# Optimization experiments

Hardware: AMD Instinct MI355X
Metric: run time of the kernel (lower is better)

## Reference

```python
import jax, jax.numpy as jnp
import numpy as np
import math

L = 8           # n_layers
DIM = 1024
H = 16          # num_heads
HD = DIM // H   # head_dim
HID = 4096      # mlp hidden
V = 32000       # vocab
B, T = 2, 1024


def setup_inputs() -> dict:
    key = jax.random.key(0)
    ks = jax.random.split(key, 10)
    s = 0.02
    inp = {
        "input_ids": jax.random.randint(ks[0], (B, T), 0, V, dtype=jnp.int32),
        "labels": jax.random.randint(ks[1], (B, T), 0, V, dtype=jnp.int32),
        "Wemb": jax.random.normal(ks[2], (V, DIM), jnp.float32) * s,   # tied embed / lm_head
        "Wq": jax.random.normal(ks[3], (L, DIM, DIM), jnp.float32) * s,
        "Wk": jax.random.normal(ks[4], (L, DIM, DIM), jnp.float32) * s,
        "Wv": jax.random.normal(ks[5], (L, DIM, DIM), jnp.float32) * s,
        "Wo": jax.random.normal(ks[6], (L, DIM, DIM), jnp.float32) * s,
        "Wfc": jax.random.normal(ks[7], (L, DIM, HID), jnp.float32) * s,
        "Wgate": jax.random.normal(ks[8], (L, DIM, HID), jnp.float32) * s,
        "Wproj": jax.random.normal(ks[9], (L, HID, DIM), jnp.float32) * s,
    }
    return inp


def _forward(input_ids, labels, Wemb, Wq, Wk, Wv, Wo, Wfc, Wgate, Wproj):
    b, t = input_ids.shape
    h = Wemb[input_ids]                                   # [B,T,C] embedding lookup
    # causal additive mask: -inf strictly above diagonal
    mask = jnp.triu(jnp.full((t, t), -jnp.inf, dtype=h.dtype), k=1)
    inv_sqrt_L = 1.0 / math.sqrt(L)
    inv_sqrt_hd = 1.0 / math.sqrt(HD)
    inv_sqrt_hid = 1.0 / math.sqrt(HID)

    def block(h, params):
        wq, wk, wv, wo, wfc, wgate, wproj = params
        # attention (explicit QK^T softmax V, as in source)
        q = (h @ wq).reshape(b, t, H, HD)
        k = (h @ wk).reshape(b, t, H, HD)
        v = (h @ wv).reshape(b, t, H, HD)
        scores = jnp.einsum("bqhd,bkhd->bhqk", q, k) * inv_sqrt_hd + mask
        probs = jax.nn.softmax(scores, axis=-1)
        attn = jnp.einsum("bhqk,bkhd->bqhd", probs, v).reshape(b, t, DIM)
        h = h + (attn @ wo) * inv_sqrt_L
        # SwiGLU MLP with 1/sqrt(hidden) scaling
        mlp = (((h @ wfc) * jax.nn.silu(h @ wgate)) * inv_sqrt_hid) @ wproj
        h = h + mlp * inv_sqrt_L
        return h, None

    h, _ = jax.lax.scan(block, h, (Wq, Wk, Wv, Wo, Wfc, Wgate, Wproj))

    logits = h @ Wemb.T                                   # tied lm_head [B,T,V]
    # cross entropy with ignore_index=-1
    lab = labels.reshape(-1)
    valid = lab != -1
    safe = jnp.where(valid, lab, 0)
    logp = jax.nn.log_softmax(logits.reshape(-1, V), axis=-1)
    nll = -jnp.take_along_axis(logp, safe[:, None], axis=-1)[:, 0]
    loss = jnp.sum(jnp.where(valid, nll, 0.0)) / jnp.maximum(jnp.sum(valid), 1)
    return logits, loss


def reference(input_ids, labels, Wemb, Wq, Wk, Wv, Wo, Wfc, Wgate, Wproj):
    return _forward(input_ids, labels, Wemb, Wq, Wk, Wv, Wo, Wfc, Wgate, Wproj)
```

## Files before the change

kernel.cpp:

```cpp
#include <hip/hip_runtime.h>
#include <hip/hip_bf16.h>
#include <math.h>

#define L_LAYERS 8
#define DIM 1024
#define NH 16
#define HD 64
#define HID 4096
#define VOCAB 32000
#define BB 2
#define TT 1024
#define MROWS (BB*TT)

typedef unsigned short u16;
typedef short short8 __attribute__((ext_vector_type(8)));
typedef float f32x4 __attribute__((ext_vector_type(4)));
typedef unsigned short us4 __attribute__((ext_vector_type(4)));
typedef unsigned short us8 __attribute__((ext_vector_type(8)));

__device__ __forceinline__ float bf2f(u16 x){
  union { unsigned int u; float f; } v; v.u = ((unsigned int)x) << 16; return v.f;
}
__device__ __forceinline__ u16 f2bf(float f){
  union { float f; unsigned int u; } v; v.f = f;
  unsigned int r = (v.u + 0x7fffu + ((v.u >> 16) & 1u)) >> 16; return (u16)r;
}

#define AS1 __attribute__((address_space(1)))
#define AS3 __attribute__((address_space(3)))
__device__ __forceinline__ void gld_lds16(const void* g, void* l){
  __builtin_amdgcn_global_load_lds((const AS1 void*)g, (AS3 void*)l, 16, 0, 0);
}

__global__ void k_embed(const int* __restrict__ ids, const float* __restrict__ Wemb,
                        float* __restrict__ h, u16* __restrict__ hb){
  int bt = blockIdx.x; long id = ids[bt];
  const float4* src = (const float4*)(Wemb + id*(long)DIM);
  float4 v = src[threadIdx.x];
  ((float4*)(h + (long)bt*DIM))[threadIdx.x] = v;
  us4 o = { f2bf(v.x), f2bf(v.y), f2bf(v.z), f2bf(v.w) };
  ((us4*)(hb + (long)bt*DIM))[threadIdx.x] = o;
}

__global__ void k_cvt(const float* __restrict__ src, u16* __restrict__ dst, long n){
  long i = ((long)blockIdx.x*256 + threadIdx.x)*8;
  if (i >= n) return;
  float4 a = ((const float4*)(src+i))[0];
  float4 b = ((const float4*)(src+i))[1];
  us4 o0 = { f2bf(a.x), f2bf(a.y), f2bf(a.z), f2bf(a.w) };
  us4 o1 = { f2bf(b.x), f2bf(b.y), f2bf(b.z), f2bf(b.w) };
  ((us4*)(dst+i))[0] = o0; ((us4*)(dst+i))[1] = o1;
}

__global__ void k_cvt_layer(const float* __restrict__ Wq, const float* __restrict__ Wk,
    const float* __restrict__ Wv, const float* __restrict__ Wo,
    const float* __restrict__ Wfc, const float* __restrict__ Wg, const float* __restrict__ Wp,
    u16* __restrict__ qkvT, u16* __restrict__ woT, u16* __restrict__ fgT, u16* __restrict__ projT)
{
  int tile = blockIdx.x;
  const float* src; u16* dst; int R, C, tr, tc;
  long rowmul = 1, rowoff = 0;
  if (tile < 1024){
    int m = tile >> 8, t2 = tile & 255;
    tr = t2 >> 4; tc = t2 & 15; R = 1024; C = 1024;
    src = (m==0)?Wq:(m==1)?Wk:(m==2)?Wv:Wo;
    dst = (m<3)? qkvT + (long)m*1024*1024 : woT;
  } else if (tile < 3072){
    int m = (tile - 1024) >> 10, t2 = (tile - 1024) & 1023;
    tr = t2 >> 6; tc = t2 & 63; R = 1024; C = 4096;
    src = m ? Wg : Wfc; dst = fgT; rowmul = 2; rowoff = m;
  } else {
    int t2 = tile - 3072;
    tr = t2 >> 4; tc = t2 & 15; R = 4096; C = 1024;
    src = Wp; dst = projT;
  }
  __shared__ float ls[64][65];
  int u = threadIdx.x;
  int rr16 = u >> 4;
  int cu   = u & 15;
  #pragma unroll
  for (int p = 0; p < 4; ++p){
    int r = p*16 + rr16;
    float4 v = *(const float4*)(src + (long)(tr*64 + r)*C + tc*64 + cu*4);
    ls[r][cu*4+0]=v.x; ls[r][cu*4+1]=v.y; ls[r][cu*4+2]=v.z; ls[r][cu*4+3]=v.w;
  }
  __syncthreads();
  int d  = u >> 2;
  int c4 = u & 3;
  long drow = (long)tc*64 + d;
  u16* dp = dst + (drow*rowmul + rowoff)*R + tr*64;
  #pragma unroll
  for (int g2 = 0; g2 < 2; ++g2){
    int e0 = (c4 + g2*4) * 8;
    us8 o;
    #pragma unroll
    for (int j=0;j<8;j++) o[j] = f2bf(ls[e0+j][d]);
    *((us8*)(dp + e0)) = o;
  }
}

template<int EPI>
__global__ __launch_bounds__(256, 2) void k_gemm(
    const u16* __restrict__ A, long lda,
    const u16* __restrict__ Bt, long ldb,
    void* __restrict__ Cp, long ldc,
    int K, int nMt, float alpha, int ksplit,
    u16* __restrict__ hbout)
{
  __shared__ u16 lsA[128*32];
  __shared__ u16 lsB[128*32];
  int nflat = gridDim.x; int w = blockIdx.x;
  if ((nflat & 7) == 0){ int q = nflat >> 3; w = (w & 7)*q + (w >> 3); }
  int perk = nflat / ksplit;
  int kc = w / perk; int w2 = w - kc*perk;
  int mtile = w2 % nMt, ntile = w2 / nMt;
  const u16* Ab = A + (long)mtile*128*lda + (long)kc*K;
  const u16* Bb = Bt + (long)ntile*128*ldb + (long)kc*K;
  int t = threadIdx.x;
  int wv = t >> 6, ln = t & 63;
  int srow = t >> 2;
  int scol = (t & 3) * 8;
  int fr = ln & 15, kg = ln >> 4;
  int wr = wv >> 1, wc = wv & 1;
  const f32x4 zero = {0.f,0.f,0.f,0.f};
  f32x4 acc[4][4];
  #pragma unroll
  for (int m=0;m<4;m++)
    #pragma unroll
    for (int n=0;n<4;n++) acc[m][n] = zero;
  const u16* ga0 = Ab + (long)srow*lda + scol;
  const u16* ga1 = Ab + (long)(srow+64)*lda + scol;
  const u16* gb0 = Bb + (long)srow*ldb + scol;
  const u16* gb1 = Bb + (long)(srow+64)*ldb + scol;
  u16* la0 = lsA + wv*512;
  u16* la1 = lsA + 2048 + wv*512;
  u16* lb0 = lsB + wv*512;
  u16* lb1 = lsB + 2048 + wv*512;
  for (int k0 = 0; k0 < K; k0 += 32){
    gld_lds16(ga0 + k0, la0);
    gld_lds16(ga1 + k0, la1);
    gld_lds16(gb0 + k0, lb0);
    gld_lds16(gb1 + k0, lb1);
    __syncthreads();
    short8 af[4], bfr[4];
    #pragma unroll
    for (int m=0;m<4;m++) af[m]  = *(const short8*)(lsA + (wr*64 + m*16 + fr)*32 + kg*8);
    #pragma unroll
    for (int n=0;n<4;n++) bfr[n] = *(const short8*)(lsB + (wc*64 + n*16 + fr)*32 + kg*8);
    #pragma unroll
    for (int m=0;m<4;m++)
      #pragma unroll
      for (int n=0;n<4;n++)
        acc[m][n] = __builtin_amdgcn_mfma_f32_16x16x32_bf16(af[m], bfr[n], acc[m][n], 0, 0, 0);
    __syncthreads();
  }
  long row0 = (long)mtile*128 + wr*64 + kg*4;
  int col0 = ntile*128 + wc*64 + fr;
  if constexpr (EPI == 0){
    u16* C = (u16*)Cp;
    #pragma unroll
    for (int m=0;m<4;m++)
      #pragma unroll
      for (int r=0;r<4;r++){
        long row = row0 + m*16 + r;
        #pragma unroll
        for (int n=0;n<4;n++) C[row*ldc + col0 + n*16] = f2bf(acc[m][n][r]);
      }
  } else if constexpr (EPI == 2){
    float* C = (float*)Cp;
    #pragma unroll
    for (int m=0;m<4;m++)
      #pragma unroll
      for (int r=0;r<4;r++){
        long row = row0 + m*16 + r;
        #pragma unroll
        for (int n=0;n<4;n++){
          long idx = row*ldc + col0 + n*16;
          float v = C[idx] + acc[m][n][r]*alpha;
          C[idx] = v;
          hbout[idx] = f2bf(v);
        }
      }
  } else {
    float* C = (float*)Cp + (long)kc*MROWS*ldc;
    #pragma unroll
    for (int m=0;m<4;m++)
      #pragma unroll
      for (int r=0;r<4;r++){
        long row = row0 + m*16 + r;
        #pragma unroll
        for (int n=0;n<4;n++) C[row*ldc + col0 + n*16] = acc[m][n][r];
      }
  }
}

template<int NS>
__global__ void k_redKn(const float* __restrict__ pK, float* __restrict__ h, u16* __restrict__ hb){
  long idx = ((long)blockIdx.x*256 + threadIdx.x)*4;
  const float aL = 0.35355339059327373f;
  float4 s = *(const float4*)(pK + idx);
  #pragma unroll
  for (int j=1;j<NS;j++){
    float4 sj = *(const float4*)(pK + idx + (long)j*MROWS*1024);
    s.x += sj.x; s.y += sj.y; s.z += sj.z; s.w += sj.w;
  }
  float4 hv = *(const float4*)(h + idx);
  float4 v;
  v.x = hv.x + s.x*aL;
  v.y = hv.y + s.y*aL;
  v.z = hv.z + s.z*aL;
  v.w = hv.w + s.w*aL;
  *(float4*)(h + idx) = v;
  us4 o = { f2bf(v.x), f2bf(v.y), f2bf(v.z), f2bf(v.w) };
  *(us4*)(hb + idx) = o;
}

#define MFMA_(va,vb,vc) __builtin_amdgcn_mfma_f32_16x16x32_bf16(va,vb,vc,0,0,0)
#define RD2(base, row, ku) (*(const short8*)((base) + (row)*64 + ((((ku) ^ ((row)&7)))<<3)))

template<int EPI>
__global__ __launch_bounds__(512, 1) void k_gemm256(
    const u16* __restrict__ A, long lda,
    const u16* __restrict__ Bt, long ldb,
    void* __restrict__ Cp, long ldc,
    int K, int nMt,
    float2* __restrict__ partials)
{
  __shared__ u16 lds[65536];
  int nwg = gridDim.x; int w = blockIdx.x;
  { int q = nwg >> 3, r8 = nwg & 7; int xcd = w & 7, lw = w >> 3;
    w = (xcd < r8 ? xcd*(q+1) : r8*(q+1) + (xcd-r8)*q) + lw; }
  int mtile = w % nMt, ntile = w / nMt;
  const u16* Abase = A + (long)mtile*256*lda;
  const u16* Bbase = Bt + (long)ntile*256*ldb;
  int tid = threadIdx.x;
  int wid = tid >> 6, ln = tid & 63;
  int wm = wid >> 2, wn = wid & 3;
  int fr = ln & 15, kg = ln >> 4;

  f32x4 acc[8][4];
  #pragma unroll
  for (int a=0;a<8;a++)
    #pragma unroll
    for (int b=0;b<4;b++) acc[a][b] = (f32x4){0.f,0.f,0.f,0.f};

#define STAGE_A(i, kofs, dstbase) do{ \
    int u_ = (i)*512 + tid; int r_ = u_>>3; int cu_ = u_&7; \
    gld_lds16(Abase + (long)r_*lda + (kofs) + ((cu_^(r_&7))<<3), \
              (dstbase) + (((i)*512 + wid*64)<<3)); }while(0)
#define STAGE_B(i, kofs, dstbase) do{ \
    int u_ = (i)*512 + tid; int r_ = u_>>3; int cu_ = u_&7; \
    gld_lds16(Bbase + (long)r_*ldb + (kofs) + ((cu_^(r_&7))<<3), \
              (dstbase) + (((i)*512 + wid*64)<<3)); }while(0)

#define KHALF(ks) do{ \
    short8 a0 = RD2(ldsA, wm*128 +   0 + fr, (ks)*4+kg); \
    short8 a1 = RD2(ldsA, wm*128 +  16 + fr, (ks)*4+kg); \
    short8 a2 = RD2(ldsA, wm*128 +  32 + fr, (ks)*4+kg); \
    short8 a3 = RD2(ldsA, wm*128 +  48 + fr, (ks)*4+kg); \
    short8 a4 = RD2(ldsA, wm*128 +  64 + fr, (ks)*4+kg); \
    short8 a5 = RD2(ldsA, wm*128 +  80 + fr, (ks)*4+kg); \
    short8 a6 = RD2(ldsA, wm*128 +  96 + fr, (ks)*4+kg); \
    short8 a7 = RD2(ldsA, wm*128 + 112 + fr, (ks)*4+kg); \
    short8 b0 = RD2(ldsB, wn*64 +  0 + fr, (ks)*4+kg); \
    short8 b1 = RD2(ldsB, wn*64 + 16 + fr, (ks)*4+kg); \
    short8 b2 = RD2(ldsB, wn*64 + 32 + fr, (ks)*4+kg); \
    short8 b3 = RD2(ldsB, wn*64 + 48 + fr, (ks)*4+kg); \
    acc[0][0]=MFMA_(a0,b0,acc[0][0]); acc[1][0]=MFMA_(a1,b0,acc[1][0]); \
    acc[0][1]=MFMA_(a0,b1,acc[0][1]); acc[1][1]=MFMA_(a1,b1,acc[1][1]); \
    acc[2][0]=MFMA_(a2,b0,acc[2][0]); acc[3][0]=MFMA_(a3,b0,acc[3][0]); \
    acc[2][1]=MFMA_(a2,b1,acc[2][1]); acc[3][1]=MFMA_(a3,b1,acc[3][1]); \
    acc[0][2]=MFMA_(a0,b2,acc[0][2]); acc[1][2]=MFMA_(a1,b2,acc[1][2]); \
    acc[0][3]=MFMA_(a0,b3,acc[0][3]); acc[1][3]=MFMA_(a1,b3,acc[1][3]); \
    acc[2][2]=MFMA_(a2,b2,acc[2][2]); acc[3][2]=MFMA_(a3,b2,acc[3][2]); \
    acc[2][3]=MFMA_(a2,b3,acc[2][3]); acc[3][3]=MFMA_(a3,b3,acc[3][3]); \
    acc[4][0]=MFMA_(a4,b0,acc[4][0]); acc[5][0]=MFMA_(a5,b0,acc[5][0]); \
    acc[4][1]=MFMA_(a4,b1,acc[4][1]); acc[5][1]=MFMA_(a5,b1,acc[5][1]); \
    acc[6][0]=MFMA_(a6,b0,acc[6][0]); acc[7][0]=MFMA_(a7,b0,acc[7][0]); \
    acc[6][1]=MFMA_(a6,b1,acc[6][1]); acc[7][1]=MFMA_(a7,b1,acc[7][1]); \
    acc[4][2]=MFMA_(a4,b2,acc[4][2]); acc[5][2]=MFMA_(a5,b2,acc[5][2]); \
    acc[4][3]=MFMA_(a4,b3,acc[4][3]); acc[5][3]=MFMA_(a5,b3,acc[5][3]); \
    acc[6][2]=MFMA_(a6,b2,acc[6][2]); acc[7][2]=MFMA_(a7,b2,acc[7][2]); \
    acc[6][3]=MFMA_(a6,b3,acc[6][3]); acc[7][3]=MFMA_(a7,b3,acc[7][3]); \
  }while(0)

  {
    u16* dA = lds; u16* dB = lds + 16384;
    STAGE_A(0, 0, dA); STAGE_A(1, 0, dA); STAGE_A(2, 0, dA); STAGE_A(3, 0, dA);
    STAGE_B(0, 0, dB); STAGE_B(1, 0, dB); STAGE_B(2, 0, dB); STAGE_B(3, 0, dB);
  }
  const int NT = K >> 6;
  #pragma unroll 2
  for (int jt = 0; jt < NT; ++jt){
    int bsel = jt & 1;
    u16* ldsA = lds + bsel*32768;
    u16* ldsB = ldsA + 16384;
    u16* nA = lds + (bsel^1)*32768;
    u16* nB = nA + 16384;
    long k1 = (long)(jt+1) << 6;
    bool pref = (jt+1 < NT);
    if (pref){
      STAGE_A(0, k1, nA); STAGE_A(1, k1, nA);
      STAGE_B(0, k1, nB); STAGE_B(1, k1, nB);
      asm volatile("s_waitcnt vmcnt(4)" ::: "memory");
    } else {
      asm volatile("s_waitcnt vmcnt(0)" ::: "memory");
    }
    __builtin_amdgcn_s_barrier();
    __builtin_amdgcn_s_setprio(1);
    KHALF(0);
    __builtin_amdgcn_s_setprio(0);
    __builtin_amdgcn_sched_barrier(0);
    if (pref){
      STAGE_A(2, k1, nA); STAGE_A(3, k1, nA);
      STAGE_B(2, k1, nB); STAGE_B(3, k1, nB);
    }
    __builtin_amdgcn_sched_barrier(0);
    __builtin_amdgcn_s_setprio(1);
    KHALF(1);
    __builtin_amdgcn_s_setprio(0);
    __builtin_amdgcn_sched_barrier(0);
    __builtin_amdgcn_s_barrier();
  }

  if constexpr (EPI == 3){
    u16* act = (u16*)Cp;
    const float sc = 0.015625f;
    #pragma unroll
    for (int a=0;a<8;a++){
      long rowb = (long)mtile*256 + wm*128 + a*16 + kg*4;
      #pragma unroll
      for (int r=0;r<4;r++){
        #pragma unroll
        for (int b=0;b<4;b++){
          float v = acc[a][b][r];
          float pv = __shfl_xor(v, 1);
          if (!(fr & 1)){
            int colg = ntile*256 + wn*64 + b*16 + fr;
            float g = pv;
            float sl = g / (1.0f + __expf(-g));
            act[(rowb+r)*ldc + (colg>>1)] = f2bf(v * sl * sc);
          }
        }
      }
    }
  } else {
    float* C = (float*)Cp;
    #pragma unroll
    for (int a=0;a<8;a++){
      long rowb = (long)mtile*256 + wm*128 + a*16 + kg*4;
      #pragma unroll
      for (int r=0;r<4;r++){
        #pragma unroll
        for (int b=0;b<4;b++){
          int colg = ntile*256 + wn*64 + b*16 + fr;
          C[(rowb+r)*ldc + colg] = acc[a][b][r];
        }
      }
    }
    float* pm = (float*)lds;
    float* ps = pm + 1024;
    #pragma unroll
    for (int a=0;a<8;a++)
      #pragma unroll
      for (int r=0;r<4;r++){
        float M = fmaxf(fmaxf(acc[a][0][r],acc[a][1][r]), fmaxf(acc[a][2][r],acc[a][3][r]));
        #pragma unroll
        for (int o=1;o<16;o<<=1) M = fmaxf(M, __shfl_xor(M, o));
        float S = __expf(acc[a][0][r]-M) + __expf(acc[a][1][r]-M)
                + __expf(acc[a][2][r]-M) + __expf(acc[a][3][r]-M);
        #pragma unroll
        for (int o=1;o<16;o<<=1) S += __shfl_xor(S, o);
        if (fr == 0){
          int rl = wm*128 + a*16 + kg*4 + r;
          pm[wn*256 + rl] = M; ps[wn*256 + rl] = S;
        }
      }
    __syncthreads();
    if (tid < 256){
      float m0 = pm[tid], m1 = pm[256+tid], m2 = pm[512+tid], m3 = pm[768+tid];
      float M = fmaxf(fmaxf(m0,m1), fmaxf(m2,m3));
      float S = ps[tid]*__expf(m0-M) + ps[256+tid]*__expf(m1-M)
              + ps[512+tid]*__expf(m2-M) + ps[768+tid]*__expf(m3-M);
      partials[((long)mtile*256 + tid)*128 + ntile] = make_float2(M, S);
    }
  }
#undef STAGE_A
#undef STAGE_B
#undef KHALF
}

__global__ void k_transpose_v(const u16* __restrict__ qkv, u16* __restrict__ vT){
  int ttile = blockIdx.x; int z = blockIdx.y;
  long b = z >> 4; int hh = z & 15;
  const u16* v = qkv + b*TT*3072 + 2048 + hh*64;
  u16* outp = vT + (long)z*64*TT;
  __shared__ u16 ls[64][65];
  int u = threadIdx.x, rr = u & 63, cc = u >> 6;
  const u16* sp = v + (long)(ttile*64 + rr)*3072 + cc*16;
  us4 a0 = ((const us4*)sp)[0];
  us4 a1 = ((const us4*)sp)[1];
  us4 a2 = ((const us4*)sp)[2];
  us4 a3 = ((const us4*)sp)[3];
  #pragma unroll
  for (int j=0;j<4;j++){ ls[rr][cc*16+j] = a0[j]; ls[rr][cc*16+4+j] = a1[j];
                         ls[rr][cc*16+8+j] = a2[j]; ls[rr][cc*16+12+j] = a3[j]; }
  __syncthreads();
  int d = u & 63;
  #pragma unroll
  for (int g=0; g<4; ++g){
    int tl = cc*16 + g*4;
    int t  = ttile*64 + tl;
    int ut = (t >> 3) & 15;
    int tp = (t & ~127) + (((ut ^ (d & 15)) << 3) | (t & 7));
    us4 o = { ls[tl+0][d], ls[tl+1][d], ls[tl+2][d], ls[tl+3][d] };
    *((us4*)(outp + (long)d*TT + tp)) = o;
  }
}

__global__ __launch_bounds__(128) void k_flash(
    const u16* __restrict__ qkv, const u16* __restrict__ vT, u16* __restrict__ attnb)
{
  __shared__ u16 lsQ[64*64];
  __shared__ u16 lsK[128*64];
  __shared__ u16 lsV[64*128];
  __shared__ u16 lsP[64*128];
  int id = blockIdx.x;
  int wq = id >> 5, z = id & 31;
  int qt = (wq < 8) ? wq : 23 - wq;
  long bT = (long)(z >> 4) * TT;
  int h64 = (z & 15) * 64;
  int t = threadIdx.x, wv = t >> 6, ln = t & 63;
  int fr = ln & 15, kg = ln >> 4;
  const u16* vbase = vT + (long)z*64*TT;

  #pragma unroll
  for (int p=0; p<4; ++p){
    int r = p*16 + wv*8 + (ln>>3);
    const u16* g = qkv + (bT + qt*64 + r)*3072 + h64 + (((ln&7) ^ (ln>>3))*8);
    gld_lds16(g, lsQ + (p*16 + wv*8)*64);
  }

  f32x4 S[2][8], O[2][4];
  float Mst[2][4], Lst[2][4];
  #pragma unroll
  for (int m=0;m<2;m++){
    #pragma unroll
    for (int n=0;n<4;n++) O[m][n] = (f32x4){0.f,0.f,0.f,0.f};
    #pragma unroll
    for (int r=0;r<4;r++){ Mst[m][r] = -3.0e38f; Lst[m][r] = 0.f; }
  }

  int nk = (qt >> 1) + 1;
  for (int kt = 0; kt < nk; ++kt){
    #pragma unroll
    for (int p=0; p<8; ++p){
      int r = p*16 + wv*8 + (ln>>3);
      const u16* g = qkv + (bT + kt*128 + r)*3072 + 1024 + h64 + (((ln&7) ^ (ln>>3))*8);
      gld_lds16(g, lsK + (p*16 + wv*8)*64);
    }
    #pragma unroll
    for (int p=0; p<8; ++p){
      int d = p*8 + wv*4 + (ln>>4);
      const u16* g = vbase + (long)d*TT + kt*128 + (ln&15)*8;
      gld_lds16(g, lsV + (p*8 + wv*4)*128);
    }
    __syncthreads();

    #pragma unroll
    for (int m=0;m<2;m++)
      #pragma unroll
      for (int n=0;n<8;n++) S[m][n] = (f32x4){0.f,0.f,0.f,0.f};
    #pragma unroll
    for (int ks=0; ks<2; ++ks){
      int un = ((ks*4 + kg) ^ (fr & 7)) * 8;
      short8 a0 = *(const short8*)(lsQ + (wv*32 +      fr)*64 + un);
      short8 a1 = *(const short8*)(lsQ + (wv*32 + 16 + fr)*64 + un);
      #pragma unroll
      for (int n=0;n<8;n++){
        short8 bb = *(const short8*)(lsK + (n*16 + fr)*64 + un);
        S[0][n] = __builtin_amdgcn_mfma_f32_16x16x32_bf16(a0, bb, S[0][n], 0,0,0);
        S[1][n] = __builtin_amdgcn_mfma_f32_16x16x32_bf16(a1, bb, S[1][n], 0,0,0);
      }
    }

    #pragma unroll
    for (int m=0;m<2;m++){
      #pragma unroll
      for (int r=0;r<4;r++){
        int rloc = wv*32 + m*16 + kg*4 + r;
        int row_g = qt*64 + rloc;
        float x[8]; float mx = -3.0e38f;
        #pragma unroll
        for (int n=0;n<8;n++){
          int col_g = kt*128 + n*16 + fr;
          x[n] = (col_g <= row_g) ? S[m][n][r]*0.125f : -3.0e38f;
          mx = fmaxf(mx, x[n]);
        }
        #pragma unroll
        for (int o=1;o<16;o<<=1) mx = fmaxf(mx, __shfl_xor(mx, o));
        float Mnew = fmaxf(Mst[m][r], mx);
        float corr = __expf(Mst[m][r] - Mnew);
        Mst[m][r] = Mnew;
        float s = 0.f;
        #pragma unroll
        for (int n=0;n<8;n++){
          float p = __expf(x[n] - Mnew);
          s += p;
          int col = n*16 + fr;
          int col2 = ((((col>>3) ^ (rloc & 15)) << 3) | (col & 7));
          lsP[rloc*128 + col2] = f2bf(p);
        }
        #pragma unroll
        for (int o=1;o<16;o<<=1) s += __shfl_xor(s, o);
        Lst[m][r] = Lst[m][r]*corr + s;
        #pragma unroll
        for (int n=0;n<4;n++) O[m][n][r] *= corr;
      }
    }

    #pragma unroll
    for (int ks=0; ks<4; ++ks){
      int up = ((ks*4 + kg) ^ fr) * 8;
      short8 p0 = *(const short8*)(lsP + (wv*32 +      fr)*128 + up);
      short8 p1 = *(const short8*)(lsP + (wv*32 + 16 + fr)*128 + up);
      #pragma unroll
      for (int n=0;n<4;n++){
        short8 vb = *(const short8*)(lsV + (n*16 + fr)*128 + up);
        O[0][n] = __builtin_amdgcn_mfma_f32_16x16x32_bf16(p0, vb, O[0][n], 0,0,0);
        O[1][n] = __builtin_amdgcn_mfma_f32_16x16x32_bf16(p1, vb, O[1][n], 0,0,0);
      }
    }
    __syncthreads();
  }

  #pragma unroll
  for (int m=0;m<2;m++)
    #pragma unroll
    for (int r=0;r<4;r++){
      float inv = 1.0f / Lst[m][r];
      long row = bT + qt*64 + wv*32 + m*16 + kg*4 + r;
      #pragma unroll
      for (int n=0;n<4;n++)
        attnb[row*1024 + h64 + n*16 + fr] = f2bf(O[m][n][r]*inv);
    }
}

__global__ void k_nll2(const float2* __restrict__ part, const float* __restrict__ logits,
                       const int* __restrict__ labels, float* __restrict__ nll){
  int row = blockIdx.x; int ln = threadIdx.x;
  const float2* pr = part + (long)row*128;
  float m = -3.0e38f, s = 0.f;
  for (int j = ln; j < 125; j += 64){
    float2 p = pr[j];
    float M = fmaxf(m, p.x);
    s = s*__expf(m - M) + p.y*__expf(p.x - M);
    m = M;
  }
  #pragma unroll
  for (int o=32;o;o>>=1){
    float om = __shfl_xor(m, o), os = __shfl_xor(s, o);
    float M = fmaxf(m, om);
    s = s*__expf(m - M) + os*__expf(om - M);
    m = M;
  }
  if (ln == 0){
    int lab = labels[row];
    float lse = m + __logf(s);
    nll[row] = (lab != -1) ? (lse - logits[(long)row*VOCAB + lab]) : 0.f;
  }
}

__global__ void k_loss(const float* __restrict__ nll, const int* __restrict__ labels,
                       float* __restrict__ out){
  int tid = threadIdx.x;
  int wv = tid >> 6;
  float s = 0.f; float c = 0.f;
  for (int i = tid; i < MROWS; i += 256){
    s += nll[i];
    c += (labels[i] != -1) ? 1.f : 0.f;
  }
  #pragma unroll
  for (int o=32;o;o>>=1){ s += __shfl_xor(s, o); c += __shfl_xor(c, o); }
  __shared__ float rsm[4], rc[4];
  if ((tid & 63) == 0){ rsm[wv] = s; rc[wv] = c; }
  __syncthreads();
  if (tid == 0){
    s = rsm[0]+rsm[1]+rsm[2]+rsm[3];
    c = rc[0]+rc[1]+rc[2]+rc[3];
    out[(long)MROWS*VOCAB] = s / fmaxf(c, 1.f);
  }
}

extern "C" void kernel_launch(void* const* d_in, const int* in_sizes, int n_in,
                              void* d_out, int out_size, void* d_ws, size_t ws_size,
                              hipStream_t stream)
{
  (void)in_sizes; (void)n_in; (void)out_size; (void)ws_size;
  const int*   ids    = (const int*)d_in[0];
  const int*   labels = (const int*)d_in[1];
  const float* Wemb   = (const float*)d_in[2];
  const float* Wq     = (const float*)d_in[3];
  const float* Wk     = (const float*)d_in[4];
  const float* Wv     = (const float*)d_in[5];
  const float* Wo     = (const float*)d_in[6];
  const float* Wfc    = (const float*)d_in[7];
  const float* Wg     = (const float*)d_in[8];
  const float* Wp     = (const float*)d_in[9];
  float* logits = (float*)d_out;

  char* ws = (char*)d_ws;
  size_t off = 0;
  auto alloc = [&](size_t bytes){ void* p = ws + off; off += (bytes + 255) & ~(size_t)255; return p; };
  u16*    wembBf = (u16*)alloc((size_t)VOCAB*DIM*2);
  float*  h      = (float*)alloc((size_t)MROWS*DIM*4);
  u16*    hb     = (u16*)alloc((size_t)MROWS*DIM*2);
  u16*    qkvT   = (u16*)alloc((size_t)3*DIM*DIM*2);
  u16*    woT    = (u16*)alloc((size_t)DIM*DIM*2);
  u16*    fgT    = (u16*)alloc((size_t)2*HID*DIM*2);
  u16*    projT  = (u16*)alloc((size_t)DIM*HID*2);
  u16*    qkv    = (u16*)alloc((size_t)MROWS*3*DIM*2);
  u16*    vT     = (u16*)alloc((size_t)BB*NH*64*TT*2);
  u16*    attnb  = (u16*)alloc((size_t)MROWS*DIM*2);
  u16*    act    = (u16*)alloc((size_t)MROWS*HID*2);
  float*  pK     = (float*)alloc((size_t)4*MROWS*DIM*4);
  float2* parts  = (float2*)alloc((size_t)MROWS*128*8);
  float*  nllb   = (float*)alloc((size_t)MROWS*4);

  dim3 blk(256,1,1);
  dim3 blk512(512,1,1);
  const float aL = 0.35355339059327373f;

  k_cvt<<<dim3(16000,1,1),blk,0,stream>>>(Wemb, wembBf, (long)VOCAB*DIM);
  k_embed<<<dim3(MROWS,1,1),blk,0,stream>>>(ids, Wemb, h, hb);

  for (int l = 0; l < L_LAYERS; ++l){
    k_cvt_layer<<<dim3(4096,1,1),blk,0,stream>>>(
        Wq + (size_t)l*DIM*DIM, Wk + (size_t)l*DIM*DIM, Wv + (size_t)l*DIM*DIM, Wo + (size_t)l*DIM*DIM,
        Wfc + (size_t)l*DIM*HID, Wg + (size_t)l*DIM*HID, Wp + (size_t)l*HID*DIM,
        qkvT, woT, fgT, projT);
    k_gemm<0><<<dim3(384,1,1),blk,0,stream>>>(hb,1024, qkvT,1024, qkv,3072,
        1024,16,1.f,1, nullptr);
    k_transpose_v<<<dim3(16,32,1),blk,0,stream>>>(qkv, vT);
    k_flash<<<dim3(512,1,1),dim3(128,1,1),0,stream>>>(qkv, vT, attnb);
    k_gemm<5><<<dim3(256,1,1),blk,0,stream>>>(attnb,1024, woT,1024, pK,1024,
        512,16,1.f,2, nullptr);
    k_redKn<2><<<dim3(2048,1,1),blk,0,stream>>>(pK, h, hb);
    k_gemm256<3><<<dim3(256,1,1),blk512,0,stream>>>(hb,1024, fgT,1024, act,4096,
        1024,8, nullptr);
    k_gemm<5><<<dim3(512,1,1),blk,0,stream>>>(act,4096, projT,4096, pK,1024,
        1024,16,1.f,4, nullptr);
    k_redKn<4><<<dim3(2048,1,1),blk,0,stream>>>(pK, h, hb);
  }
  k_gemm256<4><<<dim3(1000,1,1),blk512,0,stream>>>(hb,1024, wembBf,1024, logits,32000,
      1024,8, parts);
  k_nll2<<<dim3(MROWS,1,1),dim3(64,1,1),0,stream>>>(parts, logits, labels, nllb);
  k_loss<<<dim3(1,1,1),blk,0,stream>>>(nllb, labels, logits);
}
```

Baseline: 1.808 ms.

## Shrink flash-attention query tile to 32 rows and alias P buffer onto K

The flash attention kernel now handles 32 query rows per block instead of 64, so the grid doubles to 1024 blocks with one 16-row MFMA strip per wave. The P buffer reuses the K shared-memory region, with an extra barrier after QK^T. The goal is higher occupancy, less LDS and fewer registers per block, plus better balance of causal work across blocks. The cost is that every K/V tile is loaded twice as often, since fewer query rows share each load, and each iteration gains a synchronisation.

```diff
diff --git a/kernel.cpp b/kernel.cpp
--- a/kernel.cpp
+++ b/kernel.cpp
@@ -421,13 +421,13 @@
 __global__ __launch_bounds__(128) void k_flash(
     const u16* __restrict__ qkv, const u16* __restrict__ vT, u16* __restrict__ attnb)
 {
-  __shared__ u16 lsQ[64*64];
+  __shared__ u16 lsQ[32*64];
   __shared__ u16 lsK[128*64];
   __shared__ u16 lsV[64*128];
-  __shared__ u16 lsP[64*128];
+  u16* lsP = lsK;
   int id = blockIdx.x;
   int wq = id >> 5, z = id & 31;
-  int qt = (wq < 8) ? wq : 23 - wq;
+  int qt = (wq < 16) ? wq : 47 - wq;
   long bT = (long)(z >> 4) * TT;
   int h64 = (z & 15) * 64;
   int t = threadIdx.x, wv = t >> 6, ln = t & 63;
@@ -435,23 +435,20 @@
   const u16* vbase = vT + (long)z*64*TT;
 
   #pragma unroll
-  for (int p=0; p<4; ++p){
+  for (int p=0; p<2; ++p){
     int r = p*16 + wv*8 + (ln>>3);
-    const u16* g = qkv + (bT + qt*64 + r)*3072 + h64 + (((ln&7) ^ (ln>>3))*8);
+    const u16* g = qkv + (bT + qt*32 + r)*3072 + h64 + (((ln&7) ^ (ln>>3))*8);
     gld_lds16(g, lsQ + (p*16 + wv*8)*64);
   }
 
-  f32x4 S[2][8], O[2][4];
-  float Mst[2][4], Lst[2][4];
-  #pragma unroll
-  for (int m=0;m<2;m++){
-    #pragma unroll
-    for (int n=0;n<4;n++) O[m][n] = (f32x4){0.f,0.f,0.f,0.f};
-    #pragma unroll
-    for (int r=0;r<4;r++){ Mst[m][r] = -3.0e38f; Lst[m][r] = 0.f; }
-  }
-
-  int nk = (qt >> 1) + 1;
+  f32x4 S[8], O[4];
+  float Mst[4], Lst[4];
+  #pragma unroll
+  for (int n=0;n<4;n++) O[n] = (f32x4){0.f,0.f,0.f,0.f};
+  #pragma unroll
+  for (int r=0;r<4;r++){ Mst[r] = -3.0e38f; Lst[r] = 0.f; }
+
+  int nk = (qt >> 2) + 1;
   for (int kt = 0; kt < nk; ++kt){
     #pragma unroll
     for (int p=0; p<8; ++p){
@@ -468,82 +465,72 @@
     __syncthreads();
 
     #pragma unroll
-    for (int m=0;m<2;m++)
-      #pragma unroll
-      for (int n=0;n<8;n++) S[m][n] = (f32x4){0.f,0.f,0.f,0.f};
+    for (int n=0;n<8;n++) S[n] = (f32x4){0.f,0.f,0.f,0.f};
     #pragma unroll
     for (int ks=0; ks<2; ++ks){
       int un = ((ks*4 + kg) ^ (fr & 7)) * 8;
-      short8 a0 = *(const short8*)(lsQ + (wv*32 +      fr)*64 + un);
-      short8 a1 = *(const short8*)(lsQ + (wv*32 + 16 + fr)*64 + un);
+      short8 a0 = *(const short8*)(lsQ + (wv*16 + fr)*64 + un);
       #pragma unroll
       for (int n=0;n<8;n++){
         short8 bb = *(const short8*)(lsK + (n*16 + fr)*64 + un);
-        S[0][n] = __builtin_amdgcn_mfma_f32_16x16x32_bf16(a0, bb, S[0][n], 0,0,0);
-        S[1][n] = __builtin_amdgcn_mfma_f32_16x16x32_bf16(a1, bb, S[1][n], 0,0,0);
-      }
-    }
-
-    #pragma unroll
-    for (int m=0;m<2;m++){
-      #pragma unroll
-      for (int r=0;r<4;r++){
-        int rloc = wv*32 + m*16 + kg*4 + r;
-        int row_g = qt*64 + rloc;
-        float x[8]; float mx = -3.0e38f;
-        #pragma unroll
-        for (int n=0;n<8;n++){
-          int col_g = kt*128 + n*16 + fr;
-          x[n] = (col_g <= row_g) ? S[m][n][r]*0.125f : -3.0e38f;
-          mx = fmaxf(mx, x[n]);
-        }
-        #pragma unroll
-        for (int o=1;o<16;o<<=1) mx = fmaxf(mx, __shfl_xor(mx, o));
-        float Mnew = fmaxf(Mst[m][r], mx);
-        float corr = __expf(Mst[m][r] - Mnew);
-        Mst[m][r] = Mnew;
-        float s = 0.f;
-        #pragma unroll
-        for (int n=0;n<8;n++){
-          float p = __expf(x[n] - Mnew);
-          s += p;
-          int col = n*16 + fr;
-          int col2 = ((((col>>3) ^ (rloc & 15)) << 3) | (col & 7));
-          lsP[rloc*128 + col2] = f2bf(p);
-        }
-        #pragma unroll
-        for (int o=1;o<16;o<<=1) s += __shfl_xor(s, o);
-        Lst[m][r] = Lst[m][r]*corr + s;
-        #pragma unroll
-        for (int n=0;n<4;n++) O[m][n][r] *= corr;
-      }
+        S[n] = __builtin_amdgcn_mfma_f32_16x16x32_bf16(a0, bb, S[n], 0,0,0);
+      }
+    }
+    __syncthreads();
+
+    #pragma unroll
+    for (int r=0;r<4;r++){
+      int rloc = wv*16 + kg*4 + r;
+      int row_g = qt*32 + rloc;
+      float x[8]; float mx = -3.0e38f;
+      #pragma unroll
+      for (int n=0;n<8;n++){
+        int col_g = kt*128 + n*16 + fr;
+        x[n] = (col_g <= row_g) ? S[n][r]*0.125f : -3.0e38f;
+        mx = fmaxf(mx, x[n]);
+      }
+      #pragma unroll
+      for (int o=1;o<16;o<<=1) mx = fmaxf(mx, __shfl_xor(mx, o));
+      float Mnew = fmaxf(Mst[r], mx);
+      float corr = __expf(Mst[r] - Mnew);
+      Mst[r] = Mnew;
+      float s = 0.f;
+      #pragma unroll
+      for (int n=0;n<8;n++){
+        float p = __expf(x[n] - Mnew);
+        s += p;
+        int col = n*16 + fr;
+        int col2 = ((((col>>3) ^ (rloc & 15)) << 3) | (col & 7));
+        lsP[rloc*128 + col2] = f2bf(p);
+      }
+      #pragma unroll
+      for (int o=1;o<16;o<<=1) s += __shfl_xor(s, o);
+      Lst[r] = Lst[r]*corr + s;
+      #pragma unroll
+      for (int n=0;n<4;n++) O[n][r] *= corr;
     }
 
     #pragma unroll
     for (int ks=0; ks<4; ++ks){
       int up = ((ks*4 + kg) ^ fr) * 8;
-      short8 p0 = *(const short8*)(lsP + (wv*32 +      fr)*128 + up);
-      short8 p1 = *(const short8*)(lsP + (wv*32 + 16 + fr)*128 + up);
+      short8 p0 = *(const short8*)(lsP + (wv*16 + fr)*128 + up);
       #pragma unroll
       for (int n=0;n<4;n++){
         short8 vb = *(const short8*)(lsV + (n*16 + fr)*128 + up);
-        O[0][n] = __builtin_amdgcn_mfma_f32_16x16x32_bf16(p0, vb, O[0][n], 0,0,0);
-        O[1][n] = __builtin_amdgcn_mfma_f32_16x16x32_bf16(p1, vb, O[1][n], 0,0,0);
+        O[n] = __builtin_amdgcn_mfma_f32_16x16x32_bf16(p0, vb, O[n], 0,0,0);
       }
     }
     __syncthreads();
   }
 
   #pragma unroll
-  for (int m=0;m<2;m++)
-    #pragma unroll
-    for (int r=0;r<4;r++){
-      float inv = 1.0f / Lst[m][r];
-      long row = bT + qt*64 + wv*32 + m*16 + kg*4 + r;
-      #pragma unroll
-      for (int n=0;n<4;n++)
-        attnb[row*1024 + h64 + n*16 + fr] = f2bf(O[m][n][r]*inv);
-    }
+  for (int r=0;r<4;r++){
+    float inv = 1.0f / Lst[r];
+    long row = bT + qt*32 + wv*16 + kg*4 + r;
+    #pragma unroll
+    for (int n=0;n<4;n++)
+      attnb[row*1024 + h64 + n*16 + fr] = f2bf(O[n][r]*inv);
+  }
 }
 
 __global__ void k_nll2(const float2* __restrict__ part, const float* __restrict__ logits,
@@ -642,7 +629,7 @@
     k_gemm<0><<<dim3(384,1,1),blk,0,stream>>>(hb,1024, qkvT,1024, qkv,3072,
         1024,16,1.f,1, nullptr);
     k_transpose_v<<<dim3(16,32,1),blk,0,stream>>>(qkv, vT);
-    k_flash<<<dim3(512,1,1),dim3(128,1,1),0,stream>>>(qkv, vT, attnb);
+    k_flash<<<dim3(1024,1,1),dim3(128,1,1),0,stream>>>(qkv, vT, attnb);
     k_gemm<5><<<dim3(256,1,1),blk,0,stream>>>(attnb,1024, woT,1024, pK,1024,
         512,16,1.f,2, nullptr);
     k_redKn<2><<<dim3(2048,1,1),blk,0,stream>>>(pK, h, hb);
```

New measurement: 1.689 ms. 6.6% less time.
